# Optimization experiments

Hardware: AMD Instinct MI355X
Metric: run time of the kernel (lower is better)

## Reference

```python
import jax, jax.numpy as jnp
import numpy as np

N_TOKENS = 2097152
N_FEATURES = 64
N_MODELS = 64
N_LAYERS = 4


def setup_inputs() -> dict:
    key = jax.random.key(0)
    k1, k2, k3 = jax.random.split(key, 3)
    x = jax.random.normal(k1, (N_TOKENS, N_FEATURES), dtype=jnp.float32)
    # Packed per-model Linear params, torch convention: weight [out, in]
    scale = 1.0 / np.sqrt(N_FEATURES)
    W = jax.random.normal(k2, (N_MODELS, N_LAYERS, N_FEATURES, N_FEATURES), dtype=jnp.float32) * scale
    b = jax.random.normal(k3, (N_MODELS, N_LAYERS, N_FEATURES), dtype=jnp.float32) * scale
    return {"x": x, "W": W, "b": b}


def reference(x, W, b):
    # x: [N, d]; rows are partitioned into N_MODELS equal contiguous slices.
    # W: [M, L, d_out, d_in], b: [M, L, d_out]
    n, d = x.shape
    xg = x.reshape(N_MODELS, n // N_MODELS, d)  # [M, n_per, d]
    for l in range(N_LAYERS):
        # torch Linear: y = x @ W.T + b, per model (grouped GEMM)
        xg = jnp.einsum('mnd,mfd->mnf', xg, W[:, l]) + b[:, l][:, None, :]
        xg = jax.nn.relu(xg)
    return xg.reshape(n, d)
```

## Files before the change

kernel.cpp:

```cpp
#include <hip/hip_runtime.h>


typedef __attribute__((ext_vector_type(8))) _Float16 f16x8;
typedef __attribute__((ext_vector_type(4))) float f32x4;

#define MODELS 64
#define LAYERS 4
#define DIM 64
#define TOKS_PER_MODEL 32768
#define BLOCKS_PER_MODEL 16
#define WAVES_PER_BLOCK 4
#define TOK_PER_WAVE (TOKS_PER_MODEL / (BLOCKS_PER_MODEL * WAVES_PER_BLOCK))
#define TILES_PER_WAVE (TOK_PER_WAVE / 16)

static __device__ __forceinline__ unsigned bf16bits(float f) {
    unsigned u = __builtin_bit_cast(unsigned, f);
    return (u + 0x7fffu + ((u >> 16) & 1u)) >> 16;
}

__global__ __launch_bounds__(256, 2) void mlp4_fused(
    const float* __restrict__ x, const float* __restrict__ W,
    const float* __restrict__ b, float* __restrict__ out) {

    const int lane = threadIdx.x & 63;
    const int wave = threadIdx.x >> 6;
    const int c = lane & 15;
    const int g = lane >> 4;

    const int m   = blockIdx.x / BLOCKS_PER_MODEL;
    const int blk = blockIdx.x % BLOCKS_PER_MODEL;
    const size_t tok0 = (size_t)m * TOKS_PER_MODEL
                      + (size_t)(blk * WAVES_PER_BLOCK + wave) * TOK_PER_WAVE;

    f16x8 wf[LAYERS][4][2];
    const float* Wm = W + (size_t)m * LAYERS * DIM * DIM;
    #pragma unroll
    for (int l = 0; l < LAYERS; ++l) {
        #pragma unroll
        for (int t = 0; t < 4; ++t) {
            const float* row = Wm + ((size_t)l * DIM + (t * 16 + c)) * DIM + 4 * g;
            f32x4 c0 = *(const f32x4*)(row + 0);
            f32x4 c1 = *(const f32x4*)(row + 16);
            f32x4 c2 = *(const f32x4*)(row + 32);
            f32x4 c3 = *(const f32x4*)(row + 48);
            f16x8 a0, a1;
            #pragma unroll
            for (int e = 0; e < 4; ++e) {
                a0[e]     = (_Float16)c0[e];
                a0[4 + e] = (_Float16)c1[e];
                a1[e]     = (_Float16)c2[e];
                a1[4 + e] = (_Float16)c3[e];
            }
            wf[l][t][0] = a0;
            wf[l][t][1] = a1;
        }
    }

    unsigned bpk[LAYERS][8];
    const float* bm = b + (size_t)m * LAYERS * DIM;
    #pragma unroll
    for (int l = 0; l < LAYERS; ++l) {
        #pragma unroll
        for (int t = 0; t < 4; ++t) {
            #pragma unroll
            for (int p = 0; p < 2; ++p) {
                unsigned r0 = bf16bits(bm[l * DIM + t * 16 + 4 * g + 2 * p]);
                unsigned r1 = bf16bits(bm[l * DIM + t * 16 + 4 * g + 2 * p + 1]);
                bpk[l][t * 2 + p] = (r1 << 16) | r0;
            }
        }
    }

    const float* xp = x   + tok0 * DIM + (size_t)(c * DIM + 4 * g);
    float*       op = out + tok0 * DIM + (size_t)(c * DIM + 4 * g);

    f32x4 xr0 = *(const f32x4*)(xp + 0);
    f32x4 xr1 = *(const f32x4*)(xp + 16);
    f32x4 xr2 = *(const f32x4*)(xp + 32);
    f32x4 xr3 = *(const f32x4*)(xp + 48);

    #pragma unroll 1
    for (int tile = 0; tile < TILES_PER_WAVE; ++tile) {
        const int nxt = (tile + 1 < TILES_PER_WAVE) ? (tile + 1) : 0;
        const float* nx = xp + (size_t)nxt * 16 * DIM;
        f32x4 xn0 = *(const f32x4*)(nx + 0);
        f32x4 xn1 = *(const f32x4*)(nx + 16);
        f32x4 xn2 = *(const f32x4*)(nx + 32);
        f32x4 xn3 = *(const f32x4*)(nx + 48);

        f16x8 z0, z1;
        #pragma unroll
        for (int e = 0; e < 4; ++e) {
            z0[e]     = (_Float16)xr0[e];
            z0[4 + e] = (_Float16)xr1[e];
            z1[e]     = (_Float16)xr2[e];
            z1[4 + e] = (_Float16)xr3[e];
        }

        f32x4 acc[4];
        #pragma unroll
        for (int l = 0; l < LAYERS; ++l) {
            #pragma unroll
            for (int t = 0; t < 4; ++t) {
                unsigned p0 = bpk[l][t * 2], p1 = bpk[l][t * 2 + 1];
                acc[t][0] = __builtin_bit_cast(float, p0 << 16);
                acc[t][1] = __builtin_bit_cast(float, p0 & 0xffff0000u);
                acc[t][2] = __builtin_bit_cast(float, p1 << 16);
                acc[t][3] = __builtin_bit_cast(float, p1 & 0xffff0000u);
            }
            #pragma unroll
            for (int t = 0; t < 4; ++t)
                acc[t] = __builtin_amdgcn_mfma_f32_16x16x32_f16(wf[l][t][0], z0, acc[t], 0, 0, 0);
            #pragma unroll
            for (int t = 0; t < 4; ++t)
                acc[t] = __builtin_amdgcn_mfma_f32_16x16x32_f16(wf[l][t][1], z1, acc[t], 0, 0, 0);

            if (l < LAYERS - 1) {
                f16x8 n0, n1;
                #pragma unroll
                for (int j = 0; j < 8; ++j) {
                    n0[j] = (_Float16)fmaxf(acc[(j >> 2)    ][j & 3], 0.0f);
                    n1[j] = (_Float16)fmaxf(acc[2 + (j >> 2)][j & 3], 0.0f);
                }
                z0 = n0;
                z1 = n1;
            }
        }

        float* o = op + (size_t)tile * 16 * DIM;
        #pragma unroll
        for (int t = 0; t < 4; ++t) {
            f32x4 res;
            #pragma unroll
            for (int r = 0; r < 4; ++r) res[r] = fmaxf(acc[t][r], 0.0f);
            *(f32x4*)(o + t * 16) = res;
        }

        xr0 = xn0; xr1 = xn1; xr2 = xn2; xr3 = xn3;
    }
}

extern "C" void kernel_launch(void* const* d_in, const int* in_sizes, int n_in,
                              void* d_out, int out_size, void* d_ws, size_t ws_size,
                              hipStream_t stream) {
    (void)in_sizes; (void)n_in; (void)out_size; (void)d_ws; (void)ws_size;
    const float* x = (const float*)d_in[0];
    const float* W = (const float*)d_in[1];
    const float* b = (const float*)d_in[2];
    float* out = (float*)d_out;
    mlp4_fused<<<dim3(MODELS * BLOCKS_PER_MODEL), dim3(256), 0, stream>>>(x, W, b, out);
}
```

Measured before the change: 245.5 us.

## Stage fp16 weights and fp32 bias in LDS to raise occupancy

Weights and biases leave registers and go into shared memory. Each wave converts one layer's weights to fp16 fragments and writes them to LDS, and the MFMA loop reads them back per tile, which frees registers so launch bounds can rise from 2 to 4 blocks per CU. Bias is now kept in fp32 instead of packed bf16. The fp16 conversions switch to packed round-toward-zero cvt_pkrtz, which changes rounding slightly and adds LDS read traffic in the inner loop.

Result: slower. 629.0 us (+156.2%).

```diff
diff --git a/kernel.cpp b/kernel.cpp
--- a/kernel.cpp
+++ b/kernel.cpp
@@ -2,6 +2,7 @@
 
 
 typedef __attribute__((ext_vector_type(8))) _Float16 f16x8;
+typedef __attribute__((ext_vector_type(2))) __fp16 fp16x2;
 typedef __attribute__((ext_vector_type(4))) float f32x4;
 
 #define MODELS 64
@@ -13,14 +14,17 @@
 #define TOK_PER_WAVE (TOKS_PER_MODEL / (BLOCKS_PER_MODEL * WAVES_PER_BLOCK))
 #define TILES_PER_WAVE (TOK_PER_WAVE / 16)
 
-static __device__ __forceinline__ unsigned bf16bits(float f) {
-    unsigned u = __builtin_bit_cast(unsigned, f);
-    return (u + 0x7fffu + ((u >> 16) & 1u)) >> 16;
-}
+#define WF_BYTES (LAYERS * 4 * 2 * 64 * 16)
+#define BIAS_OFF WF_BYTES
+#define LDS_BYTES (WF_BYTES + LAYERS * DIM * 4)
 
-__global__ __launch_bounds__(256, 2) void mlp4_fused(
+union H8 { f16x8 v; fp16x2 h2[4]; };
+
+__global__ __launch_bounds__(256, 4) void mlp4_fused(
     const float* __restrict__ x, const float* __restrict__ W,
     const float* __restrict__ b, float* __restrict__ out) {
+
+    __shared__ __align__(16) unsigned char smem[LDS_BYTES];
 
     const int lane = threadIdx.x & 63;
     const int wave = threadIdx.x >> 6;
@@ -32,44 +36,33 @@
     const size_t tok0 = (size_t)m * TOKS_PER_MODEL
                       + (size_t)(blk * WAVES_PER_BLOCK + wave) * TOK_PER_WAVE;
 
-    f16x8 wf[LAYERS][4][2];
-    const float* Wm = W + (size_t)m * LAYERS * DIM * DIM;
-    #pragma unroll
-    for (int l = 0; l < LAYERS; ++l) {
+    {
+        const int l = wave;
+        const float* Wl = W + ((size_t)m * LAYERS + l) * DIM * DIM;
         #pragma unroll
         for (int t = 0; t < 4; ++t) {
-            const float* row = Wm + ((size_t)l * DIM + (t * 16 + c)) * DIM + 4 * g;
+            const float* row = Wl + (size_t)(t * 16 + c) * DIM + 4 * g;
             f32x4 c0 = *(const f32x4*)(row + 0);
             f32x4 c1 = *(const f32x4*)(row + 16);
             f32x4 c2 = *(const f32x4*)(row + 32);
             f32x4 c3 = *(const f32x4*)(row + 48);
-            f16x8 a0, a1;
+            H8 a0, a1;
             #pragma unroll
             for (int e = 0; e < 4; ++e) {
-                a0[e]     = (_Float16)c0[e];
-                a0[4 + e] = (_Float16)c1[e];
-                a1[e]     = (_Float16)c2[e];
-                a1[4 + e] = (_Float16)c3[e];
+                a0.v[e]     = (_Float16)c0[e];
+                a0.v[4 + e] = (_Float16)c1[e];
+                a1.v[e]     = (_Float16)c2[e];
+                a1.v[4 + e] = (_Float16)c3[e];
             }
-            wf[l][t][0] = a0;
-            wf[l][t][1] = a1;
+            *(f16x8*)(smem + ((size_t)((l * 4 + t) * 2 + 0) * 1024) + lane * 16) = a0.v;
+            *(f16x8*)(smem + ((size_t)((l * 4 + t) * 2 + 1) * 1024) + lane * 16) = a1.v;
+        }
+        if (lane < 16) {
+            const float* bl = b + ((size_t)m * LAYERS + l) * DIM + lane * 4;
+            *(f32x4*)(smem + BIAS_OFF + l * 256 + lane * 16) = *(const f32x4*)bl;
         }
     }
-
-    unsigned bpk[LAYERS][8];
-    const float* bm = b + (size_t)m * LAYERS * DIM;
-    #pragma unroll
-    for (int l = 0; l < LAYERS; ++l) {
-        #pragma unroll
-        for (int t = 0; t < 4; ++t) {
-            #pragma unroll
-            for (int p = 0; p < 2; ++p) {
-                unsigned r0 = bf16bits(bm[l * DIM + t * 16 + 4 * g + 2 * p]);
-                unsigned r1 = bf16bits(bm[l * DIM + t * 16 + 4 * g + 2 * p + 1]);
-                bpk[l][t * 2 + p] = (r1 << 16) | r0;
-            }
-        }
-    }
+    __syncthreads();
 
     const float* xp = x   + tok0 * DIM + (size_t)(c * DIM + 4 * g);
     float*       op = out + tok0 * DIM + (size_t)(c * DIM + 4 * g);
@@ -88,42 +81,49 @@
         f32x4 xn2 = *(const f32x4*)(nx + 32);
         f32x4 xn3 = *(const f32x4*)(nx + 48);
 
-        f16x8 z0, z1;
-        #pragma unroll
-        for (int e = 0; e < 4; ++e) {
-            z0[e]     = (_Float16)xr0[e];
-            z0[4 + e] = (_Float16)xr1[e];
-            z1[e]     = (_Float16)xr2[e];
-            z1[4 + e] = (_Float16)xr3[e];
-        }
+        H8 z0u, z1u;
+        z0u.h2[0] = __builtin_amdgcn_cvt_pkrtz(xr0[0], xr0[1]);
+        z0u.h2[1] = __builtin_amdgcn_cvt_pkrtz(xr0[2], xr0[3]);
+        z0u.h2[2] = __builtin_amdgcn_cvt_pkrtz(xr1[0], xr1[1]);
+        z0u.h2[3] = __builtin_amdgcn_cvt_pkrtz(xr1[2], xr1[3]);
+        z1u.h2[0] = __builtin_amdgcn_cvt_pkrtz(xr2[0], xr2[1]);
+        z1u.h2[1] = __builtin_amdgcn_cvt_pkrtz(xr2[2], xr2[3]);
+        z1u.h2[2] = __builtin_amdgcn_cvt_pkrtz(xr3[0], xr3[1]);
+        z1u.h2[3] = __builtin_amdgcn_cvt_pkrtz(xr3[2], xr3[3]);
+        f16x8 z0 = z0u.v, z1 = z1u.v;
 
         f32x4 acc[4];
         #pragma unroll
         for (int l = 0; l < LAYERS; ++l) {
             #pragma unroll
+            for (int t = 0; t < 4; ++t)
+                acc[t] = *(const f32x4*)(smem + BIAS_OFF + l * 256 + t * 64 + g * 16);
+            #pragma unroll
             for (int t = 0; t < 4; ++t) {
-                unsigned p0 = bpk[l][t * 2], p1 = bpk[l][t * 2 + 1];
-                acc[t][0] = __builtin_bit_cast(float, p0 << 16);
-                acc[t][1] = __builtin_bit_cast(float, p0 & 0xffff0000u);
-                acc[t][2] = __builtin_bit_cast(float, p1 << 16);
-                acc[t][3] = __builtin_bit_cast(float, p1 & 0xffff0000u);
+                f16x8 w0 = *(const f16x8*)(smem + ((size_t)((l * 4 + t) * 2 + 0) * 1024) + lane * 16);
+                acc[t] = __builtin_amdgcn_mfma_f32_16x16x32_f16(w0, z0, acc[t], 0, 0, 0);
             }
             #pragma unroll
-            for (int t = 0; t < 4; ++t)
-                acc[t] = __builtin_amdgcn_mfma_f32_16x16x32_f16(wf[l][t][0], z0, acc[t], 0, 0, 0);
-            #pragma unroll
-            for (int t = 0; t < 4; ++t)
-                acc[t] = __builtin_amdgcn_mfma_f32_16x16x32_f16(wf[l][t][1], z1, acc[t], 0, 0, 0);
+            for (int t = 0; t < 4; ++t) {
+                f16x8 w1 = *(const f16x8*)(smem + ((size_t)((l * 4 + t) * 2 + 1) * 1024) + lane * 16);
+                acc[t] = __builtin_amdgcn_mfma_f32_16x16x32_f16(w1, z1, acc[t], 0, 0, 0);
+            }
 
             if (l < LAYERS - 1) {
-                f16x8 n0, n1;
+                H8 n0, n1;
                 #pragma unroll
-                for (int j = 0; j < 8; ++j) {
-                    n0[j] = (_Float16)fmaxf(acc[(j >> 2)    ][j & 3], 0.0f);
-                    n1[j] = (_Float16)fmaxf(acc[2 + (j >> 2)][j & 3], 0.0f);
+                for (int t = 0; t < 2; ++t) {
+                    n0.h2[t * 2 + 0] = __builtin_amdgcn_cvt_pkrtz(
+                        fmaxf(acc[t][0], 0.0f), fmaxf(acc[t][1], 0.0f));
+                    n0.h2[t * 2 + 1] = __builtin_amdgcn_cvt_pkrtz(
+                        fmaxf(acc[t][2], 0.0f), fmaxf(acc[t][3], 0.0f));
+                    n1.h2[t * 2 + 0] = __builtin_amdgcn_cvt_pkrtz(
+                        fmaxf(acc[2 + t][0], 0.0f), fmaxf(acc[2 + t][1], 0.0f));
+                    n1.h2[t * 2 + 1] = __builtin_amdgcn_cvt_pkrtz(
+                        fmaxf(acc[2 + t][2], 0.0f), fmaxf(acc[2 + t][3], 0.0f));
                 }
-                z0 = n0;
-                z1 = n1;
+                z0 = n0.v;
+                z1 = n1.v;
             }
         }
 
```
